# Kernel optimization log

Hardware: AMD Instinct MI355X
Metric: run time of the kernel (lower is better)

The kernel has to match this reference:

```python
import jax, jax.numpy as jnp
import numpy as np

TWO_PI = 2.0 * np.pi
LN_EPS = 1e-5


def _gelu(x):
    return jax.nn.gelu(x, approximate=False)


def _layer_norm(h):
    mu = jnp.mean(h, axis=-1, keepdims=True)
    var = jnp.mean(jnp.square(h - mu), axis=-1, keepdims=True)
    return (h - mu) * jax.lax.rsqrt(var + LN_EPS)


def _torsion_field(x, W, b, tf, tc):
    # x: [B, in], W: [out, in], tf: [order, out, in], tc: scalar
    base = x @ W.T + b
    corr = jnp.zeros_like(base)
    order = tf.shape[0]
    for n in range(order):
        lo = x @ tf[n].T  # [B, out]
        phase = TWO_PI * (n + 1) * lo / (jnp.mean(jnp.abs(lo)) + 1e-8)
        corr = corr + jnp.sin(phase) * lo / (n + 1)
    return base + jax.nn.sigmoid(tc) * corr


def setup_inputs() -> dict:
    key = jax.random.key(0)
    ks = jax.random.split(key, 16)
    B, D_IN, D_R, D_I, D_O, D_H = 2097152, 6, 4, 16, 4, 8
    ts = 0.1
    inp = {
        "x": jax.random.normal(ks[0], (B, D_IN), dtype=jnp.float32),
        # input_projection
        "W_in": jax.random.normal(ks[1], (D_R, D_IN), dtype=jnp.float32) * 0.1,
        "b_in": jnp.zeros((D_R,), jnp.float32),
        # layer1_reciprocal (MiniTorsionField, order=2)
        "r_w": jax.random.normal(ks[2], (D_R, D_R), dtype=jnp.float32) * 0.1,
        "r_b": jnp.zeros((D_R,), jnp.float32),
        "r_tf": jax.random.normal(ks[3], (2, D_R, D_R), dtype=jnp.float32) * ts,
        "r_tc": jnp.float32(0.5),
        # layer1_internal (MiniTorsionField, order=3, strength*0.8)
        "i_w": jax.random.normal(ks[4], (D_I, D_I), dtype=jnp.float32) * 0.1,
        "i_b": jnp.zeros((D_I,), jnp.float32),
        "i_tf": jax.random.normal(ks[5], (3, D_I, D_I), dtype=jnp.float32) * (ts * 0.8),
        "i_tc": jnp.float32(0.5),
        # cross flows
        "W_ri": jax.random.normal(ks[6], (D_I, D_R), dtype=jnp.float32) * 0.1,
        "b_ri": jnp.zeros((D_I,), jnp.float32),
        "W_ir": jax.random.normal(ks[7], (D_R, D_I), dtype=jnp.float32) * 0.1,
        "b_ir": jnp.zeros((D_R,), jnp.float32),
        "flow_gate": jnp.float32(0.5),
        "mem": jax.random.normal(ks[8], (1, D_I), dtype=jnp.float32) * 0.01,
        # output projection: Linear(4,8) -> GELU -> Linear(8,4)
        "W_o1": jax.random.normal(ks[9], (D_H, D_R), dtype=jnp.float32) * 0.1,
        "b_o1": jnp.zeros((D_H,), jnp.float32),
        "W_o2": jax.random.normal(ks[10], (D_O, D_H), dtype=jnp.float32) * 0.1,
        "b_o2": jnp.zeros((D_O,), jnp.float32),
    }
    return inp


def reference(x, W_in, b_in, r_w, r_b, r_tf, r_tc, i_w, i_b, i_tf, i_tc,
              W_ri, b_ri, W_ir, b_ir, flow_gate, mem, W_o1, b_o1, W_o2, b_o2):
    B = x.shape[0]
    x_recip = _gelu(x @ W_in.T + b_in)                      # [B, 4]
    x_internal = jnp.broadcast_to(mem, (B, mem.shape[1]))   # [B, 16]

    h_r = _gelu(_layer_norm(_torsion_field(x_recip, r_w, r_b, r_tf, r_tc)))
    h_i = _gelu(_layer_norm(_torsion_field(x_internal, i_w, i_b, i_tf, i_tc)))

    gate = jax.nn.sigmoid(flow_gate)
    h_i = h_i + gate * (h_r @ W_ri.T + b_ri)
    h_r = h_r + gate * (h_i @ W_ir.T + b_ir)

    out = _gelu(h_r @ W_o1.T + b_o1) @ W_o2.T + b_o2        # [B, 4]
    return out
```

## Files before the change

### kernel.cpp

```cpp
#include <hip/hip_runtime.h>
#include <math.h>

#define TWO_PI_F 6.2831853071795864769f
#define LUT_N    2048
#define LUT_SCALE 170.66666667f
#define LUT_STEP  0.005859375f

static __device__ __forceinline__ float sin_rev(float x) {
#if __has_builtin(__builtin_amdgcn_sinf)
    return __builtin_amdgcn_sinf(x);
#else
    return __sinf(TWO_PI_F * x);
#endif
}

static __device__ __forceinline__ float cdf_acc(float v) {
    const float y  = v * 0.70710678118654752f;
    const float ay = fabsf(y);
    const float t  = __builtin_amdgcn_rcpf(fmaf(0.3275911f, ay, 1.0f));
    const float e  = __builtin_amdgcn_exp2f(y * y * -1.4426950408889634f);
    float p = fmaf(1.061405429f, t, -1.453152027f);
    p = fmaf(p, t, 1.421413741f);
    p = fmaf(p, t, -0.284496736f);
    p = fmaf(p, t, 0.254829592f);
    const float erf_abs = 1.0f - p * t * e;
    const float erf_v   = __builtin_copysignf(erf_abs, v);
    return fmaf(0.5f, erf_v, 0.5f);
}

static __device__ __forceinline__ float gelu_s(float v) { return v * cdf_acc(v); }

static __device__ __forceinline__ float gelu_lut(float x, const float2* __restrict__ lut) {
    float f = fminf(fmaxf(fmaf(x, LUT_SCALE, 1024.0f), 0.0f), 2047.5f);
    float ff = floorf(f);
    float fr = f - ff;
    float2 e = lut[(int)ff];
    return x * fmaf(fr, e.y, e.x);
}

static __device__ __forceinline__ void build_lut(float2* lut, int tid) {
    for (int i = tid; i < LUT_N; i += 256) {
        float x0 = fmaf((float)i, LUT_STEP, -6.0f);
        float t0 = cdf_acc(x0);
        float t1 = cdf_acc(x0 + LUT_STEP);
        lut[i] = make_float2(t0, t1 - t0);
    }
}

__global__ __launch_bounds__(256, 8) void k_sum(
    const float* __restrict__ x,
    const float* __restrict__ W_in, const float* __restrict__ b_in,
    const float* __restrict__ r_tf,
    float2* __restrict__ partials, int B)
{
    const int tid = threadIdx.x;
    __shared__ float2 s_lut[LUT_N];
    __shared__ float s_red[8];
    build_lut(s_lut, tid);
    __syncthreads();

    const int npairs = B >> 1;
    const int TT = gridDim.x * blockDim.x;
    const int gtid = blockIdx.x * blockDim.x + tid;
    float s0 = 0.f, s1 = 0.f;

    for (int p = gtid; p < npairs; p += TT) {
        const float4* xp = (const float4*)(x + (size_t)p * 12);
        float4 q0 = xp[0], q1 = xp[1], q2 = xp[2];
        float xv[2][6] = {{q0.x, q0.y, q0.z, q0.w, q1.x, q1.y},
                          {q1.z, q1.w, q2.x, q2.y, q2.z, q2.w}};
#pragma unroll
        for (int r = 0; r < 2; ++r) {
            float xr[4];
#pragma unroll
            for (int j = 0; j < 4; ++j) {
                float a = b_in[j];
#pragma unroll
                for (int k = 0; k < 6; ++k) a = fmaf(W_in[j*6+k], xv[r][k], a);
                xr[j] = gelu_lut(a, s_lut);
            }
#pragma unroll
            for (int j = 0; j < 4; ++j) {
                float l0 = 0.f, l1 = 0.f;
#pragma unroll
                for (int k = 0; k < 4; ++k) {
                    l0 = fmaf(r_tf[j*4+k],      xr[k], l0);
                    l1 = fmaf(r_tf[16 + j*4+k], xr[k], l1);
                }
                s0 += fabsf(l0);
                s1 += fabsf(l1);
            }
        }
    }
    if ((B & 1) && gtid == 0) {
        const float* xs = x + (size_t)(B-1) * 6;
        float xr[4];
#pragma unroll
        for (int j = 0; j < 4; ++j) {
            float a = b_in[j];
#pragma unroll
            for (int k = 0; k < 6; ++k) a = fmaf(W_in[j*6+k], xs[k], a);
            xr[j] = gelu_lut(a, s_lut);
        }
#pragma unroll
        for (int j = 0; j < 4; ++j) {
            float l0 = 0.f, l1 = 0.f;
#pragma unroll
            for (int k = 0; k < 4; ++k) {
                l0 = fmaf(r_tf[j*4+k],      xr[k], l0);
                l1 = fmaf(r_tf[16 + j*4+k], xr[k], l1);
            }
            s0 += fabsf(l0);
            s1 += fabsf(l1);
        }
    }
#pragma unroll
    for (int off = 32; off > 0; off >>= 1) {
        s0 += __shfl_down(s0, off);
        s1 += __shfl_down(s1, off);
    }
    if ((tid & 63) == 0) { s_red[(tid>>6)*2] = s0; s_red[(tid>>6)*2+1] = s1; }
    __syncthreads();
    if (tid == 0) {
        partials[blockIdx.x] = make_float2(s_red[0]+s_red[2]+s_red[4]+s_red[6],
                                           s_red[1]+s_red[3]+s_red[5]+s_red[7]);
    }
}

__global__ __launch_bounds__(256) void k_mid(
    const float2* __restrict__ partials, int nb, int B,
    const float* __restrict__ i_w,  const float* __restrict__ i_b,
    const float* __restrict__ i_tf, const float* __restrict__ i_tc,
    const float* __restrict__ W_ri, const float* __restrict__ b_ri,
    const float* __restrict__ W_ir, const float* __restrict__ b_ir,
    const float* __restrict__ flow_gate, const float* __restrict__ mem,
    const float* __restrict__ W_o1, const float* __restrict__ b_o1,
    const float* __restrict__ r_tf, const float* __restrict__ r_tc,
    float* __restrict__ cst)
{
    const int tid = threadIdx.x;
    __shared__ float s_red[8], s_hc[16], s_cv[4], s_m4[16];

    float t0 = 0.f, t1 = 0.f;
    for (int k = tid; k < nb; k += 256) {
        const float2 pr = partials[k];
        t0 += pr.x; t1 += pr.y;
    }
#pragma unroll
    for (int off = 32; off > 0; off >>= 1) {
        t0 += __shfl_down(t0, off);
        t1 += __shfl_down(t1, off);
    }
    if ((tid & 63) == 0) { s_red[(tid>>6)*2] = t0; s_red[(tid>>6)*2+1] = t1; }
    __syncthreads();
    const float sr = 1.0f / (1.0f + expf(-r_tc[0]));
    if (tid == 0) {
        const float u0 = s_red[0]+s_red[2]+s_red[4]+s_red[6];
        const float u1 = s_red[1]+s_red[3]+s_red[5]+s_red[7];
        const float m0 = u0 / (4.0f * (float)B);
        const float m1 = u1 / (4.0f * (float)B);
        cst[0] = 1.0f / ((m0 + 1e-8f) * sr);
        cst[1] = 4.0f / ((m1 + 1e-8f) * sr);
    }

    if (tid < 64) {
        const int j = tid & 15;
        float base = i_b[j];
#pragma unroll
        for (int k = 0; k < 16; ++k) base = fmaf(i_w[j*16 + k], mem[k], base);
        float corr = 0.f;
#pragma unroll
        for (int n = 0; n < 3; ++n) {
            float lo = 0.f;
#pragma unroll
            for (int k = 0; k < 16; ++k) lo = fmaf(i_tf[n*256 + j*16 + k], mem[k], lo);
            float a = fabsf(lo);
            a += __shfl_xor(a, 1); a += __shfl_xor(a, 2);
            a += __shfl_xor(a, 4); a += __shfl_xor(a, 8);
            const float mean = a * (1.0f/16.0f);
            const float phase = TWO_PI_F * (float)(n+1) * lo / (mean + 1e-8f);
            corr = fmaf(sinf(phase), lo / (float)(n+1), corr);
        }
        const float sc = 1.0f / (1.0f + expf(-i_tc[0]));
        const float t = fmaf(sc, corr, base);
        float mu = t;
        mu += __shfl_xor(mu, 1); mu += __shfl_xor(mu, 2);
        mu += __shfl_xor(mu, 4); mu += __shfl_xor(mu, 8);
        mu *= (1.0f/16.0f);
        const float d = t - mu;
        float v = d*d;
        v += __shfl_xor(v, 1); v += __shfl_xor(v, 2);
        v += __shfl_xor(v, 4); v += __shfl_xor(v, 8);
        v *= (1.0f/16.0f);
        const float h = gelu_s(d * rsqrtf(v + 1e-5f));
        if (tid < 16) s_hc[j] = h;
    }
    __syncthreads();
    const float g = 1.0f / (1.0f + expf(-flow_gate[0]));
    if (tid < 4) {
        float acc = 0.f;
#pragma unroll
        for (int m = 0; m < 16; ++m)
            acc = fmaf(W_ir[tid*16 + m], fmaf(g, b_ri[m], s_hc[m]), acc);
        s_cv[tid] = g * (acc + b_ir[tid]);
    }
    if (tid < 16) {
        const int l = tid >> 2, j = tid & 3;
        float M = 0.f;
#pragma unroll
        for (int m = 0; m < 16; ++m) M = fmaf(W_ir[l*16 + m], W_ri[m*4 + j], M);
        s_m4[tid] = g * g * M;
        cst[8  + tid] = sr * r_tf[tid];
        cst[24 + tid] = 0.5f * sr * r_tf[16 + tid];
    }
    __syncthreads();
    if (tid < 32) {
        const int h = tid >> 2, j = tid & 3;
        float we = 0.f;
#pragma unroll
        for (int l = 0; l < 4; ++l)
            we = fmaf(W_o1[h*4 + l], ((l == j) ? 1.0f : 0.0f) + s_m4[l*4 + j], we);
        cst[40 + tid] = we;
    }
    if (tid < 8) {
        float be = b_o1[tid];
#pragma unroll
        for (int l = 0; l < 4; ++l) be = fmaf(W_o1[tid*4 + l], s_cv[l], be);
        cst[72 + tid] = be;
    }
}

__global__ __launch_bounds__(256, 4) void k_main(
    const float* __restrict__ x,
    const float* __restrict__ W_in, const float* __restrict__ b_in,
    const float* __restrict__ r_w,  const float* __restrict__ r_b,
    const float* __restrict__ W_o2, const float* __restrict__ b_o2,
    const float* __restrict__ cst,
    float* __restrict__ out, int B)
{
    const int tid = threadIdx.x;
    __shared__ float2 s_lut[LUT_N];
    build_lut(s_lut, tid);
    __syncthreads();

    const float C0 = cst[0], C1 = cst[1];

    const int npairs = B >> 1;
    const int TT = gridDim.x * blockDim.x;
    const int gtid = blockIdx.x * blockDim.x + tid;

    for (int p = gtid; p < npairs; p += TT) {
        const float4* xp = (const float4*)(x + (size_t)p * 12);
        float4 q0 = xp[0], q1 = xp[1], q2 = xp[2];
        float xv[2][6] = {{q0.x, q0.y, q0.z, q0.w, q1.x, q1.y},
                          {q1.z, q1.w, q2.x, q2.y, q2.z, q2.w}};
#pragma unroll
        for (int r = 0; r < 2; ++r) {
            float xr[4];
#pragma unroll
            for (int j = 0; j < 4; ++j) {
                float a = b_in[j];
#pragma unroll
                for (int k = 0; k < 6; ++k) a = fmaf(W_in[j*6+k], xv[r][k], a);
                xr[j] = gelu_lut(a, s_lut);
            }
            float t[4];
#pragma unroll
            for (int j = 0; j < 4; ++j) {
                float L0 = 0.f, L1 = 0.f, bse = r_b[j];
#pragma unroll
                for (int k = 0; k < 4; ++k) {
                    L0  = fmaf(cst[8  + j*4+k], xr[k], L0);
                    L1  = fmaf(cst[24 + j*4+k], xr[k], L1);
                    bse = fmaf(r_w[j*4+k],      xr[k], bse);
                }
                t[j] = fmaf(sin_rev(C0*L0), L0, fmaf(sin_rev(C1*L1), L1, bse));
            }
            const float mu = 0.25f * (t[0] + t[1] + t[2] + t[3]);
            float d0 = t[0]-mu, d1 = t[1]-mu, d2 = t[2]-mu, d3 = t[3]-mu;
            float var = fmaf(d0, d0, fmaf(d1, d1, fmaf(d2, d2, d3*d3)));
            const float inv = __builtin_amdgcn_rsqf(fmaf(0.25f, var, 1e-5f));
            float hr[4] = { gelu_lut(d0*inv, s_lut), gelu_lut(d1*inv, s_lut),
                            gelu_lut(d2*inv, s_lut), gelu_lut(d3*inv, s_lut) };

            float hid[8];
#pragma unroll
            for (int h = 0; h < 8; ++h) {
                float a = cst[72 + h];
#pragma unroll
                for (int j = 0; j < 4; ++j) a = fmaf(cst[40 + h*4+j], hr[j], a);
                hid[h] = gelu_lut(a, s_lut);
            }
            float o[4];
#pragma unroll
            for (int oo = 0; oo < 4; ++oo) {
                float a = b_o2[oo];
#pragma unroll
                for (int h = 0; h < 8; ++h) a = fmaf(W_o2[oo*8+h], hid[h], a);
                o[oo] = a;
            }
            float* op = out + (size_t)8*p + (size_t)4*r;
            __builtin_nontemporal_store(o[0], op + 0);
            __builtin_nontemporal_store(o[1], op + 1);
            __builtin_nontemporal_store(o[2], op + 2);
            __builtin_nontemporal_store(o[3], op + 3);
        }
    }

    if ((B & 1) && gtid == 0) {
        const float* xs = x + (size_t)(B-1) * 6;
        float xr[4];
#pragma unroll
        for (int j = 0; j < 4; ++j) {
            float a = b_in[j];
#pragma unroll
            for (int k = 0; k < 6; ++k) a = fmaf(W_in[j*6+k], xs[k], a);
            xr[j] = gelu_lut(a, s_lut);
        }
        float t[4];
#pragma unroll
        for (int j = 0; j < 4; ++j) {
            float L0 = 0.f, L1 = 0.f, bse = r_b[j];
#pragma unroll
            for (int k = 0; k < 4; ++k) {
                L0  = fmaf(cst[8  + j*4+k], xr[k], L0);
                L1  = fmaf(cst[24 + j*4+k], xr[k], L1);
                bse = fmaf(r_w[j*4+k],      xr[k], bse);
            }
            t[j] = fmaf(sin_rev(C0*L0), L0, fmaf(sin_rev(C1*L1), L1, bse));
        }
        const float mu = 0.25f * (t[0]+t[1]+t[2]+t[3]);
        float d0=t[0]-mu, d1=t[1]-mu, d2=t[2]-mu, d3=t[3]-mu;
        const float var = 0.25f * (d0*d0 + d1*d1 + d2*d2 + d3*d3);
        const float inv = __builtin_amdgcn_rsqf(var + 1e-5f);
        float hr[4] = { gelu_lut(d0*inv, s_lut), gelu_lut(d1*inv, s_lut),
                        gelu_lut(d2*inv, s_lut), gelu_lut(d3*inv, s_lut) };
        float hid[8];
#pragma unroll
        for (int h = 0; h < 8; ++h) {
            float a = cst[72 + h];
#pragma unroll
            for (int j = 0; j < 4; ++j) a = fmaf(cst[40 + h*4+j], hr[j], a);
            hid[h] = gelu_lut(a, s_lut);
        }
        float o[4];
#pragma unroll
        for (int oo = 0; oo < 4; ++oo) {
            float a = b_o2[oo];
#pragma unroll
            for (int h = 0; h < 8; ++h) a = fmaf(W_o2[oo*8+h], hid[h], a);
            o[oo] = a;
        }
        ((float4*)out)[(size_t)B - 1] = make_float4(o[0], o[1], o[2], o[3]);
    }
}

extern "C" void kernel_launch(void* const* d_in, const int* in_sizes, int n_in,
                              void* d_out, int out_size, void* d_ws, size_t ws_size,
                              hipStream_t stream)
{
    const float* x    = (const float*)d_in[0];
    const float* W_in = (const float*)d_in[1];
    const float* b_in = (const float*)d_in[2];
    const float* r_w  = (const float*)d_in[3];
    const float* r_b  = (const float*)d_in[4];
    const float* r_tf = (const float*)d_in[5];
    const float* r_tc = (const float*)d_in[6];
    const float* i_w  = (const float*)d_in[7];
    const float* i_b  = (const float*)d_in[8];
    const float* i_tf = (const float*)d_in[9];
    const float* i_tc = (const float*)d_in[10];
    const float* W_ri = (const float*)d_in[11];
    const float* b_ri = (const float*)d_in[12];
    const float* W_ir = (const float*)d_in[13];
    const float* b_ir = (const float*)d_in[14];
    const float* fg   = (const float*)d_in[15];
    const float* mem  = (const float*)d_in[16];
    const float* W_o1 = (const float*)d_in[17];
    const float* b_o1 = (const float*)d_in[18];
    const float* W_o2 = (const float*)d_in[19];
    const float* b_o2 = (const float*)d_in[20];
    float* out = (float*)d_out;
    float* ws  = (float*)d_ws;

    const int B = in_sizes[0] / 6;

    int NB1 = 1024;
    const long cap = (long)(ws_size / 4) - 128;
    if (cap < 2L * NB1) NB1 = (int)(cap / 2);
    if (NB1 < 1) NB1 = 1;
    float*  cst      = ws;
    float2* partials = (float2*)(ws + 128);

    k_sum<<<NB1, 256, 0, stream>>>(x, W_in, b_in, r_tf, partials, B);

    k_mid<<<1, 256, 0, stream>>>(partials, NB1, B, i_w, i_b, i_tf, i_tc,
                                 W_ri, b_ri, W_ir, b_ir, fg, mem, W_o1, b_o1,
                                 r_tf, r_tc, cst);

    int NB2 = 2048;
    const int npairs = B >> 1;
    if (NB2 * 256 > npairs + 255) NB2 = (npairs + 255) / 256;
    if (NB2 < 1) NB2 = 1;
    k_main<<<NB2, 256, 0, stream>>>(x, W_in, b_in, r_w, r_b, W_o2, b_o2,
                                    cst, out, B);
}
```

Measured before the change: 46.90 us.

## Remove mid kernel by folding its work into sum and main kernels

The single-block k_mid launch is removed. Its constant-folding work (internal torsion branch, cross-flow matrices, output weights) now runs in block 0 of k_sum, and the final reduction of partial sums runs redundantly in every k_main block. This removes one kernel launch and the serial gap it creates. It also raises k_sum's grid to 2048 blocks, lowers k_main's grid to 1536 with a higher occupancy hint, and writes outputs as float4 nontemporal stores. The cost is that every main block re-reads all 2048 partials before it starts.

```diff
diff --git a/kernel.cpp b/kernel.cpp
--- a/kernel.cpp
+++ b/kernel.cpp
@@ -27,7 +27,6 @@
     const float erf_v   = __builtin_copysignf(erf_abs, v);
     return fmaf(0.5f, erf_v, 0.5f);
 }
-
 static __device__ __forceinline__ float gelu_s(float v) { return v * cdf_acc(v); }
 
 static __device__ __forceinline__ float gelu_lut(float x, const float2* __restrict__ lut) {
@@ -50,13 +49,89 @@
 __global__ __launch_bounds__(256, 8) void k_sum(
     const float* __restrict__ x,
     const float* __restrict__ W_in, const float* __restrict__ b_in,
-    const float* __restrict__ r_tf,
-    float2* __restrict__ partials, int B)
+    const float* __restrict__ r_tf, const float* __restrict__ r_tc,
+    const float* __restrict__ i_w,  const float* __restrict__ i_b,
+    const float* __restrict__ i_tf, const float* __restrict__ i_tc,
+    const float* __restrict__ W_ri, const float* __restrict__ b_ri,
+    const float* __restrict__ W_ir, const float* __restrict__ b_ir,
+    const float* __restrict__ flow_gate, const float* __restrict__ mem,
+    const float* __restrict__ W_o1, const float* __restrict__ b_o1,
+    float2* __restrict__ partials, float* __restrict__ cst, int B)
 {
     const int tid = threadIdx.x;
     __shared__ float2 s_lut[LUT_N];
-    __shared__ float s_red[8];
+    __shared__ float s_red[8], s_hc[16], s_cv[4], s_m4[16];
     build_lut(s_lut, tid);
+
+    if (blockIdx.x == 0) {
+        if (tid < 64) {
+            const int j = tid & 15;
+            float base = i_b[j];
+#pragma unroll
+            for (int k = 0; k < 16; ++k) base = fmaf(i_w[j*16 + k], mem[k], base);
+            float corr = 0.f;
+#pragma unroll
+            for (int n = 0; n < 3; ++n) {
+                float lo = 0.f;
+#pragma unroll
+                for (int k = 0; k < 16; ++k) lo = fmaf(i_tf[n*256 + j*16 + k], mem[k], lo);
+                float a = fabsf(lo);
+                a += __shfl_xor(a, 1); a += __shfl_xor(a, 2);
+                a += __shfl_xor(a, 4); a += __shfl_xor(a, 8);
+                const float mean = a * (1.0f/16.0f);
+                const float phase = TWO_PI_F * (float)(n+1) * lo / (mean + 1e-8f);
+                corr = fmaf(sinf(phase), lo / (float)(n+1), corr);
+            }
+            const float sc = 1.0f / (1.0f + expf(-i_tc[0]));
+            const float t = fmaf(sc, corr, base);
+            float mu = t;
+            mu += __shfl_xor(mu, 1); mu += __shfl_xor(mu, 2);
+            mu += __shfl_xor(mu, 4); mu += __shfl_xor(mu, 8);
+            mu *= (1.0f/16.0f);
+            const float d = t - mu;
+            float v = d*d;
+            v += __shfl_xor(v, 1); v += __shfl_xor(v, 2);
+            v += __shfl_xor(v, 4); v += __shfl_xor(v, 8);
+            v *= (1.0f/16.0f);
+            const float h = gelu_s(d * rsqrtf(v + 1e-5f));
+            if (tid < 16) s_hc[j] = h;
+        }
+        __syncthreads();
+        const float g  = 1.0f / (1.0f + expf(-flow_gate[0]));
+        const float sr = 1.0f / (1.0f + expf(-r_tc[0]));
+        if (tid < 4) {
+            float acc = 0.f;
+#pragma unroll
+            for (int m = 0; m < 16; ++m)
+                acc = fmaf(W_ir[tid*16 + m], fmaf(g, b_ri[m], s_hc[m]), acc);
+            s_cv[tid] = g * (acc + b_ir[tid]);
+        }
+        if (tid < 16) {
+            const int l = tid >> 2, j = tid & 3;
+            float M = 0.f;
+#pragma unroll
+            for (int m = 0; m < 16; ++m) M = fmaf(W_ir[l*16 + m], W_ri[m*4 + j], M);
+            s_m4[tid] = g * g * M;
+            cst[8  + tid] = sr * r_tf[tid];
+            cst[24 + tid] = 0.5f * sr * r_tf[16 + tid];
+        }
+        if (tid == 0) cst[2] = sr;
+        __syncthreads();
+        if (tid < 32) {
+            const int h = tid >> 2, j = tid & 3;
+            float we = 0.f;
+#pragma unroll
+            for (int l = 0; l < 4; ++l)
+                we = fmaf(W_o1[h*4 + l], ((l == j) ? 1.0f : 0.0f) + s_m4[l*4 + j], we);
+            cst[40 + tid] = we;
+        }
+        if (tid < 8) {
+            float be = b_o1[tid];
+#pragma unroll
+            for (int l = 0; l < 4; ++l) be = fmaf(W_o1[tid*4 + l], s_cv[l], be);
+            cst[72 + tid] = be;
+        }
+    }
     __syncthreads();
 
     const int npairs = B >> 1;
@@ -127,123 +202,44 @@
     }
 }
 
-__global__ __launch_bounds__(256) void k_mid(
-    const float2* __restrict__ partials, int nb, int B,
-    const float* __restrict__ i_w,  const float* __restrict__ i_b,
-    const float* __restrict__ i_tf, const float* __restrict__ i_tc,
-    const float* __restrict__ W_ri, const float* __restrict__ b_ri,
-    const float* __restrict__ W_ir, const float* __restrict__ b_ir,
-    const float* __restrict__ flow_gate, const float* __restrict__ mem,
-    const float* __restrict__ W_o1, const float* __restrict__ b_o1,
-    const float* __restrict__ r_tf, const float* __restrict__ r_tc,
-    float* __restrict__ cst)
-{
-    const int tid = threadIdx.x;
-    __shared__ float s_red[8], s_hc[16], s_cv[4], s_m4[16];
-
-    float t0 = 0.f, t1 = 0.f;
-    for (int k = tid; k < nb; k += 256) {
-        const float2 pr = partials[k];
-        t0 += pr.x; t1 += pr.y;
-    }
-#pragma unroll
-    for (int off = 32; off > 0; off >>= 1) {
-        t0 += __shfl_down(t0, off);
-        t1 += __shfl_down(t1, off);
-    }
-    if ((tid & 63) == 0) { s_red[(tid>>6)*2] = t0; s_red[(tid>>6)*2+1] = t1; }
-    __syncthreads();
-    const float sr = 1.0f / (1.0f + expf(-r_tc[0]));
-    if (tid == 0) {
-        const float u0 = s_red[0]+s_red[2]+s_red[4]+s_red[6];
-        const float u1 = s_red[1]+s_red[3]+s_red[5]+s_red[7];
-        const float m0 = u0 / (4.0f * (float)B);
-        const float m1 = u1 / (4.0f * (float)B);
-        cst[0] = 1.0f / ((m0 + 1e-8f) * sr);
-        cst[1] = 4.0f / ((m1 + 1e-8f) * sr);
-    }
-
-    if (tid < 64) {
-        const int j = tid & 15;
-        float base = i_b[j];
-#pragma unroll
-        for (int k = 0; k < 16; ++k) base = fmaf(i_w[j*16 + k], mem[k], base);
-        float corr = 0.f;
-#pragma unroll
-        for (int n = 0; n < 3; ++n) {
-            float lo = 0.f;
-#pragma unroll
-            for (int k = 0; k < 16; ++k) lo = fmaf(i_tf[n*256 + j*16 + k], mem[k], lo);
-            float a = fabsf(lo);
-            a += __shfl_xor(a, 1); a += __shfl_xor(a, 2);
-            a += __shfl_xor(a, 4); a += __shfl_xor(a, 8);
-            const float mean = a * (1.0f/16.0f);
-            const float phase = TWO_PI_F * (float)(n+1) * lo / (mean + 1e-8f);
-            corr = fmaf(sinf(phase), lo / (float)(n+1), corr);
-        }
-        const float sc = 1.0f / (1.0f + expf(-i_tc[0]));
-        const float t = fmaf(sc, corr, base);
-        float mu = t;
-        mu += __shfl_xor(mu, 1); mu += __shfl_xor(mu, 2);
-        mu += __shfl_xor(mu, 4); mu += __shfl_xor(mu, 8);
-        mu *= (1.0f/16.0f);
-        const float d = t - mu;
-        float v = d*d;
-        v += __shfl_xor(v, 1); v += __shfl_xor(v, 2);
-        v += __shfl_xor(v, 4); v += __shfl_xor(v, 8);
-        v *= (1.0f/16.0f);
-        const float h = gelu_s(d * rsqrtf(v + 1e-5f));
-        if (tid < 16) s_hc[j] = h;
-    }
-    __syncthreads();
-    const float g = 1.0f / (1.0f + expf(-flow_gate[0]));
-    if (tid < 4) {
-        float acc = 0.f;
-#pragma unroll
-        for (int m = 0; m < 16; ++m)
-            acc = fmaf(W_ir[tid*16 + m], fmaf(g, b_ri[m], s_hc[m]), acc);
-        s_cv[tid] = g * (acc + b_ir[tid]);
-    }
-    if (tid < 16) {
-        const int l = tid >> 2, j = tid & 3;
-        float M = 0.f;
-#pragma unroll
-        for (int m = 0; m < 16; ++m) M = fmaf(W_ir[l*16 + m], W_ri[m*4 + j], M);
-        s_m4[tid] = g * g * M;
-        cst[8  + tid] = sr * r_tf[tid];
-        cst[24 + tid] = 0.5f * sr * r_tf[16 + tid];
-    }
-    __syncthreads();
-    if (tid < 32) {
-        const int h = tid >> 2, j = tid & 3;
-        float we = 0.f;
-#pragma unroll
-        for (int l = 0; l < 4; ++l)
-            we = fmaf(W_o1[h*4 + l], ((l == j) ? 1.0f : 0.0f) + s_m4[l*4 + j], we);
-        cst[40 + tid] = we;
-    }
-    if (tid < 8) {
-        float be = b_o1[tid];
-#pragma unroll
-        for (int l = 0; l < 4; ++l) be = fmaf(W_o1[tid*4 + l], s_cv[l], be);
-        cst[72 + tid] = be;
-    }
-}
-
-__global__ __launch_bounds__(256, 4) void k_main(
+__global__ __launch_bounds__(256, 6) void k_main(
     const float* __restrict__ x,
     const float* __restrict__ W_in, const float* __restrict__ b_in,
     const float* __restrict__ r_w,  const float* __restrict__ r_b,
     const float* __restrict__ W_o2, const float* __restrict__ b_o2,
+    const float2* __restrict__ partials, int nb,
     const float* __restrict__ cst,
     float* __restrict__ out, int B)
 {
     const int tid = threadIdx.x;
     __shared__ float2 s_lut[LUT_N];
+    __shared__ float s_red[8];
+    __shared__ float s_c[2];
     build_lut(s_lut, tid);
+
+    float t0 = 0.f, t1 = 0.f;
+    for (int k = tid; k < nb; k += 256) {
+        const float2 pr = partials[k];
+        t0 += pr.x; t1 += pr.y;
+    }
+#pragma unroll
+    for (int off = 32; off > 0; off >>= 1) {
+        t0 += __shfl_down(t0, off);
+        t1 += __shfl_down(t1, off);
+    }
+    if ((tid & 63) == 0) { s_red[(tid>>6)*2] = t0; s_red[(tid>>6)*2+1] = t1; }
     __syncthreads();
-
-    const float C0 = cst[0], C1 = cst[1];
+    if (tid == 0) {
+        const float sr = cst[2];
+        const float u0 = s_red[0]+s_red[2]+s_red[4]+s_red[6];
+        const float u1 = s_red[1]+s_red[3]+s_red[5]+s_red[7];
+        const float m0 = u0 / (4.0f * (float)B);
+        const float m1 = u1 / (4.0f * (float)B);
+        s_c[0] = 1.0f / ((m0 + 1e-8f) * sr);
+        s_c[1] = 4.0f / ((m1 + 1e-8f) * sr);
+    }
+    __syncthreads();
+    const float C0 = s_c[0], C1 = s_c[1];
 
     const int npairs = B >> 1;
     const int TT = gridDim.x * blockDim.x;
@@ -254,6 +250,7 @@
         float4 q0 = xp[0], q1 = xp[1], q2 = xp[2];
         float xv[2][6] = {{q0.x, q0.y, q0.z, q0.w, q1.x, q1.y},
                           {q1.z, q1.w, q2.x, q2.y, q2.z, q2.w}};
+        float o2[2][4];
 #pragma unroll
         for (int r = 0; r < 2; ++r) {
             float xr[4];
@@ -291,20 +288,19 @@
                 for (int j = 0; j < 4; ++j) a = fmaf(cst[40 + h*4+j], hr[j], a);
                 hid[h] = gelu_lut(a, s_lut);
             }
-            float o[4];
 #pragma unroll
             for (int oo = 0; oo < 4; ++oo) {
                 float a = b_o2[oo];
 #pragma unroll
                 for (int h = 0; h < 8; ++h) a = fmaf(W_o2[oo*8+h], hid[h], a);
-                o[oo] = a;
-            }
-            float* op = out + (size_t)8*p + (size_t)4*r;
-            __builtin_nontemporal_store(o[0], op + 0);
-            __builtin_nontemporal_store(o[1], op + 1);
-            __builtin_nontemporal_store(o[2], op + 2);
-            __builtin_nontemporal_store(o[3], op + 3);
-        }
+                o2[r][oo] = a;
+            }
+        }
+        typedef float v4f __attribute__((ext_vector_type(4)));
+        v4f r0 = (v4f){ o2[0][0], o2[0][1], o2[0][2], o2[0][3] };
+        v4f r1 = (v4f){ o2[1][0], o2[1][1], o2[1][2], o2[1][3] };
+        __builtin_nontemporal_store(r0, (v4f*)out + (size_t)2*p);
+        __builtin_nontemporal_store(r1, (v4f*)out + (size_t)2*p + 1);
     }
 
     if ((B & 1) && gtid == 0) {
@@ -384,24 +380,22 @@
     float* ws  = (float*)d_ws;
 
     const int B = in_sizes[0] / 6;
-
-    int NB1 = 1024;
+    const int npairs = B >> 1;
+
+    int NB1 = 2048;
     const long cap = (long)(ws_size / 4) - 128;
     if (cap < 2L * NB1) NB1 = (int)(cap / 2);
     if (NB1 < 1) NB1 = 1;
     float*  cst      = ws;
     float2* partials = (float2*)(ws + 128);
 
-    k_sum<<<NB1, 256, 0, stream>>>(x, W_in, b_in, r_tf, partials, B);
-
-    k_mid<<<1, 256, 0, stream>>>(partials, NB1, B, i_w, i_b, i_tf, i_tc,
-                                 W_ri, b_ri, W_ir, b_ir, fg, mem, W_o1, b_o1,
-                                 r_tf, r_tc, cst);
-
-    int NB2 = 2048;
-    const int npairs = B >> 1;
+    k_sum<<<NB1, 256, 0, stream>>>(x, W_in, b_in, r_tf, r_tc, i_w, i_b, i_tf, i_tc,
+                                   W_ri, b_ri, W_ir, b_ir, fg, mem, W_o1, b_o1,
+                                   partials, cst, B);
+
+    int NB2 = 1536;
     if (NB2 * 256 > npairs + 255) NB2 = (npairs + 255) / 256;
     if (NB2 < 1) NB2 = 1;
     k_main<<<NB2, 256, 0, stream>>>(x, W_in, b_in, r_w, r_b, W_o2, b_o2,
-                                    cst, out, B);
-}
+                                    partials, NB1, cst, out, B);
+}
```

Result: faster. 43.11 us (median of 2 runs) (-8.1%).
